# Performance work log

Measured on AMD Instinct MI355X. Metric: run time of the kernel, lower is better.

The kernel has to match this reference:

```python
import jax, jax.numpy as jnp
import numpy as np

N = 100000   # nodes
E = 640000   # edges
DIN = 128
DOUT = 128
BN_EPS = 1e-5


def setup_inputs() -> dict:
    key = jax.random.key(0)
    k = jax.random.split(key, 6)
    x = jax.random.normal(k[0], (N, DIN), dtype=jnp.float32)
    edge_index = jax.random.randint(k[1], (2, E), 0, N, dtype=jnp.int64)
    # MLP params: Linear(DIN,DOUT) -> BatchNorm1d(DOUT) -> ReLU -> Linear(DOUT,DOUT)
    s1 = 1.0 / np.sqrt(DIN)
    s2 = 1.0 / np.sqrt(DOUT)
    W1 = jax.random.uniform(k[2], (DIN, DOUT), jnp.float32, -s1, s1)
    b1 = jax.random.uniform(k[3], (DOUT,), jnp.float32, -s1, s1)
    gamma = jnp.ones((DOUT,), jnp.float32)
    beta = jnp.zeros((DOUT,), jnp.float32)
    W2 = jax.random.uniform(k[4], (DOUT, DOUT), jnp.float32, -s2, s2)
    b2 = jax.random.uniform(k[5], (DOUT,), jnp.float32, -s2, s2)
    eps = jnp.zeros((), jnp.float32)  # train_eps=True, init 0.0
    return {"x": x, "edge_index": edge_index, "W1": W1, "b1": b1,
            "gamma": gamma, "beta": beta, "W2": W2, "b2": b2, "eps": eps}


def reference(x, edge_index, W1, b1, gamma, beta, W2, b2, eps):
    src = edge_index[0]
    dst = edge_index[1]
    # GIN sum aggregation: gather source features, scatter-add to target nodes
    agg = jax.ops.segment_sum(x[src], dst, num_segments=N)  # [N, DIN]
    h = agg + (1.0 + eps) * x  # eps-weighted residual combine
    # MLP: Linear -> BatchNorm1d (training stats, biased var) -> ReLU -> Linear
    h = h @ W1 + b1  # [N, DOUT]
    mu = jnp.mean(h, axis=0)
    var = jnp.mean((h - mu) ** 2, axis=0)
    h = (h - mu) * jax.lax.rsqrt(var + BN_EPS) * gamma + beta
    h = jnp.maximum(h, 0.0)
    return h @ W2 + b2
```

## Files before the change

kernel.cpp:

```cpp
#include <hip/hip_runtime.h>

#define N_NODES 100000
#define DIM     128
#define NEDGE   640000
#define BN_EPS  1e-5f

#define PB_CNT  2500
#define PB_X    6250
#define PB_W    64

#define NSLOT   32
#define NBUCKET 64
#define T_TILES 4
#define GGRID   1563
#define AGRID   6250

typedef __bf16 bf16x8 __attribute__((ext_vector_type(8)));
typedef float  f32x4  __attribute__((ext_vector_type(4)));
typedef unsigned short u16x8 __attribute__((ext_vector_type(8)));

__device__ __forceinline__ unsigned short f2b(float f) {
    unsigned u = __builtin_bit_cast(unsigned, f);
    u += 0x7fffu + ((u >> 16) & 1u);
    return (unsigned short)(u >> 16);
}
__device__ __forceinline__ float b2f(unsigned short b) {
    return __builtin_bit_cast(float, ((unsigned)b) << 16);
}

__global__ __launch_bounds__(256) void k_prep(const float* __restrict__ x,
                                              const float* __restrict__ W1,
                                              const float* __restrict__ W2,
                                              const int* __restrict__ ei,
                                              unsigned short* __restrict__ xb,
                                              unsigned short* __restrict__ Wt1,
                                              unsigned short* __restrict__ Wt2,
                                              unsigned* __restrict__ cnt,
                                              int* __restrict__ slots) {
    const int b = blockIdx.x;
    const int t = threadIdx.x;
    if (b < PB_CNT) {
        int e = b * 256 + t;
        int src = ei[e];
        int dst = ei[NEDGE + e];
        unsigned r = (unsigned)e & 3u;
        #pragma unroll
        for (int a = 0; a < 4; ++a) {
            unsigned rk = atomicAdd(&cnt[dst * 4 + r], 1u);
            if (rk < 8u) {
                slots[dst * NSLOT + r * 8 + rk] = src;
                break;
            }
            r = (r + 1) & 3u;
        }
    } else if (b < PB_CNT + PB_X) {
        size_t base = ((size_t)(b - PB_CNT) * 256 + t) * 8;
        float4 v0 = *(const float4*)(x + base);
        float4 v1 = *(const float4*)(x + base + 4);
        u16x8 o;
        o[0] = f2b(v0.x); o[1] = f2b(v0.y); o[2] = f2b(v0.z); o[3] = f2b(v0.w);
        o[4] = f2b(v1.x); o[5] = f2b(v1.y); o[6] = f2b(v1.z); o[7] = f2b(v1.w);
        *(u16x8*)(xb + base) = o;
    } else if (b < PB_CNT + PB_X + PB_W) {
        int idx = (b - PB_CNT - PB_X) * 256 + t;
        int k = idx >> 7, n = idx & 127;
        Wt1[n * 128 + k] = f2b(W1[idx]);
    } else {
        int idx = (b - PB_CNT - PB_X - PB_W) * 256 + t;
        int k = idx >> 7, n = idx & 127;
        Wt2[n * 128 + k] = f2b(W2[idx]);
    }
}

__global__ __launch_bounds__(256) void k_agg1(const unsigned short* __restrict__ xb,
                                              const unsigned* __restrict__ cnt,
                                              const int* __restrict__ slots,
                                              const float* __restrict__ epsp,
                                              const unsigned short* __restrict__ Wt,
                                              const float* __restrict__ b1,
                                              unsigned short* __restrict__ hB,
                                              float* __restrict__ buckets) {
    __shared__ __align__(16) unsigned short At[16 * 136];
    __shared__ __align__(16) unsigned short stage[4][512];
    const int t = threadIdx.x;
    const int w = t >> 6;
    const int lane = t & 63;
    const int n15 = lane & 15;
    const int quad = lane >> 4;
    const int c8 = n15 * 8;
    const int gbase = lane & 48;

    const int row0 = blockIdx.x * 16;
    const int node = row0 + w * 4 + quad;

    int4 Bfr[2][4];
    const unsigned short* wp = Wt + (w * 32 + n15) * 128 + quad * 8;
    #pragma unroll
    for (int c = 0; c < 2; ++c)
        #pragma unroll
        for (int ks = 0; ks < 4; ++ks)
            Bfr[c][ks] = *(const int4*)(wp + c * 16 * 128 + ks * 32);
    float bias[2] = { b1[w * 32 + n15], b1[w * 32 + 16 + n15] };
    const float scale = 1.0f + epsp[0];

    const uint4 cw = *(const uint4*)(cnt + node * 4);
    const int s_lo = slots[node * NSLOT + n15];
    const int s_hi = slots[node * NSLOT + 16 + n15];
    float acc[8];
    {
        u16x8 v = *(const u16x8*)(xb + (size_t)node * 128 + c8);
        #pragma unroll
        for (int j = 0; j < 8; ++j) acc[j] = scale * b2f(v[j]);
    }
    unsigned m;
    {
        unsigned d0 = cw.x > 8u ? 8u : cw.x;
        unsigned d1 = cw.y > 8u ? 8u : cw.y;
        unsigned d2 = cw.z > 8u ? 8u : cw.z;
        unsigned d3 = cw.w > 8u ? 8u : cw.w;
        m = ((1u << d0) - 1u) | (((1u << d1) - 1u) << 8) |
            (((1u << d2) - 1u) << 16) | (((1u << d3) - 1u) << 24);
    }
    const int navail = __popc(m);
    unsigned mm = m;
    int pk = 0;
    for (int done = 0; done < navail; done += 8) {
        int4 va[8];
        #pragma unroll
        for (int k = 0; k < 8; ++k) {
            if (mm) { pk = (int)__builtin_ctz(mm); mm &= (mm - 1); }
            int vlo = __shfl(s_lo, gbase + (pk & 15));
            int vhi = __shfl(s_hi, gbase + (pk & 15));
            int srck = (pk & 16) ? vhi : vlo;
            va[k] = *(const int4*)(xb + (size_t)srck * 128 + c8);
        }
        const int rem = navail - done;
        #pragma unroll
        for (int k = 0; k < 8; ++k) {
            if (k < rem) {
                u16x8 v = __builtin_bit_cast(u16x8, va[k]);
                #pragma unroll
                for (int j = 0; j < 8; ++j) acc[j] += b2f(v[j]);
            }
        }
    }
    {
        u16x8 o;
        #pragma unroll
        for (int j = 0; j < 8; ++j) o[j] = f2b(acc[j]);
        *(u16x8*)(At + (w * 4 + quad) * 136 + c8) = o;
    }
    __syncthreads();

    f32x4 accm[2] = {};
    #pragma unroll
    for (int ks = 0; ks < 4; ++ks) {
        int4 araw = *(const int4*)(At + n15 * 136 + ks * 32 + quad * 8);
        bf16x8 af = __builtin_bit_cast(bf16x8, araw);
        #pragma unroll
        for (int c = 0; c < 2; ++c)
            accm[c] = __builtin_amdgcn_mfma_f32_16x16x32_bf16(
                af, __builtin_bit_cast(bf16x8, Bfr[c][ks]), accm[c], 0, 0, 0);
    }
    float s[2] = {0.f, 0.f}, q[2] = {0.f, 0.f};
    unsigned short* st = stage[w];
    #pragma unroll
    for (int c = 0; c < 2; ++c)
        #pragma unroll
        for (int r = 0; r < 4; ++r) {
            float v = accm[c][r] + bias[c];
            s[c] += v; q[c] += v * v;
            st[(quad * 4 + r) * 32 + c * 16 + n15] = f2b(v);
        }
    {
        int so = lane * 8;
        int r = so >> 5, cc = so & 31;
        *(int4*)(hB + (size_t)(row0 + r) * 128 + w * 32 + cc) = *(const int4*)(st + so);
    }

    #pragma unroll
    for (int c = 0; c < 2; ++c) {
        s[c] += __shfl_down(s[c], 32); q[c] += __shfl_down(q[c], 32);
        s[c] += __shfl_down(s[c], 16); q[c] += __shfl_down(q[c], 16);
    }
    if (quad == 0) {
        float* bk = buckets + (blockIdx.x & (NBUCKET - 1)) * 256;
        atomicAdd(&bk[w * 32 + n15], s[0]);
        atomicAdd(&bk[w * 32 + 16 + n15], s[1]);
        atomicAdd(&bk[128 + w * 32 + n15], q[0]);
        atomicAdd(&bk[128 + w * 32 + 16 + n15], q[1]);
    }
}

__global__ __launch_bounds__(256) void k_gemm2(const unsigned short* __restrict__ hb,
                                               const unsigned short* __restrict__ Wt2,
                                               const float* __restrict__ buckets,
                                               const float* __restrict__ gamma,
                                               const float* __restrict__ beta,
                                               const float* __restrict__ b2,
                                               float* __restrict__ out) {
    __shared__ __align__(16) unsigned short Asb[2][16 * 136];
    __shared__ __align__(16) float stage[4][512];
    __shared__ __align__(16) float aff_s[256];
    const int t = threadIdx.x;
    const int w = t >> 6;
    const int lane = t & 63;
    const int n15 = lane & 15;
    const int quad = lane >> 4;
    const int kb = w * 32 + quad * 8;

    const int tile0 = blockIdx.x * T_TILES;
    int4 gr;
    {
        int r0 = tile0 * 16;
        if (r0 < N_NODES)
            gr = *(const int4*)(hb + (size_t)(r0 + n15) * 128 + kb);
    }

    int4 Bfr[2][4];
    const unsigned short* wp = Wt2 + (w * 32 + n15) * 128 + quad * 8;
    #pragma unroll
    for (int c = 0; c < 2; ++c)
        #pragma unroll
        for (int ks = 0; ks < 4; ++ks)
            Bfr[c][ks] = *(const int4*)(wp + c * 16 * 128 + ks * 32);
    float bias[2] = { b2[w * 32 + n15], b2[w * 32 + 16 + n15] };

    if (t < 128) {
        float s = 0.f, q = 0.f;
        #pragma unroll 8
        for (int b = 0; b < NBUCKET; ++b) {
            s += buckets[b * 256 + t];
            q += buckets[b * 256 + 128 + t];
        }
        float mu  = s * (1.0f / N_NODES);
        float var = q * (1.0f / N_NODES) - mu * mu;
        float a = gamma[t] * rsqrtf(var + BN_EPS);
        aff_s[t] = a;
        aff_s[128 + t] = beta[t] - mu * a;
    }
    __syncthreads();

    float akr[8], bkr[8];
    *(float4*)(akr)     = *(const float4*)(aff_s + kb);
    *(float4*)(akr + 4) = *(const float4*)(aff_s + kb + 4);
    *(float4*)(bkr)     = *(const float4*)(aff_s + 128 + kb);
    *(float4*)(bkr + 4) = *(const float4*)(aff_s + 128 + kb + 4);

    float* st = stage[w];

    #pragma unroll
    for (int i = 0; i < T_TILES; ++i) {
        const int row0 = (tile0 + i) * 16;
        const bool valid = row0 < N_NODES;
        unsigned short* al = Asb[i & 1];
        if (valid) {
            u16x8 ar = __builtin_bit_cast(u16x8, gr);
            u16x8 pr;
            #pragma unroll
            for (int j = 0; j < 8; ++j)
                pr[j] = f2b(fmaxf(fmaf(b2f(ar[j]), akr[j], bkr[j]), 0.f));
            *(int4*)(al + n15 * 136 + kb) = __builtin_bit_cast(int4, pr);
        }
        if (i + 1 < T_TILES) {
            int rn = (tile0 + i + 1) * 16;
            if (rn < N_NODES)
                gr = *(const int4*)(hb + (size_t)(rn + n15) * 128 + kb);
        }
        __syncthreads();
        if (valid) {
            f32x4 acc[2] = {};
            #pragma unroll
            for (int ks = 0; ks < 4; ++ks) {
                int4 araw = *(const int4*)(al + n15 * 136 + ks * 32 + quad * 8);
                bf16x8 af = __builtin_bit_cast(bf16x8, araw);
                #pragma unroll
                for (int c = 0; c < 2; ++c)
                    acc[c] = __builtin_amdgcn_mfma_f32_16x16x32_bf16(
                        af, __builtin_bit_cast(bf16x8, Bfr[c][ks]), acc[c], 0, 0, 0);
            }
            #pragma unroll
            for (int c = 0; c < 2; ++c)
                #pragma unroll
                for (int r = 0; r < 4; ++r)
                    st[(quad * 4 + r) * 32 + c * 16 + n15] = acc[c][r] + bias[c];
            #pragma unroll
            for (int p = 0; p < 2; ++p) {
                int fo = p * 256 + lane * 4;
                int r = fo >> 5, cc = fo & 31;
                *(float4*)(out + (size_t)(row0 + r) * 128 + w * 32 + cc) =
                    *(const float4*)(st + fo);
            }
        }
    }
}

extern "C" void kernel_launch(void* const* d_in, const int* in_sizes, int n_in,
                              void* d_out, int out_size, void* d_ws, size_t ws_size,
                              hipStream_t stream) {
    const float* x     = (const float*)d_in[0];
    const int*   ei    = (const int*)d_in[1];
    const float* W1    = (const float*)d_in[2];
    const float* b1    = (const float*)d_in[3];
    const float* gamma = (const float*)d_in[4];
    const float* beta  = (const float*)d_in[5];
    const float* W2    = (const float*)d_in[6];
    const float* b2    = (const float*)d_in[7];
    const float* eps   = (const float*)d_in[8];
    float* out = (float*)d_out;

    float* buckets      = (float*)d_ws;
    unsigned* cnt       = (unsigned*)(buckets + NBUCKET * 256);
    unsigned short* hB  = (unsigned short*)(cnt + 4 * N_NODES);
    unsigned short* xb  = hB + (size_t)N_NODES * DIM;
    unsigned short* Wt1 = xb + (size_t)N_NODES * DIM;
    unsigned short* Wt2 = Wt1 + 16384;
    int* slots          = (int*)(Wt2 + 16384);

    hipMemsetAsync(buckets, 0,
                   NBUCKET * 256 * sizeof(float) + 4 * N_NODES * sizeof(unsigned),
                   stream);

    k_prep<<<PB_CNT + PB_X + 2 * PB_W, 256, 0, stream>>>(x, W1, W2, ei, xb, Wt1, Wt2,
                                                         cnt, slots);
    k_agg1<<<AGRID, 256, 0, stream>>>(xb, cnt, slots, eps, Wt1, b1, hB, buckets);
    k_gemm2<<<GGRID, 256, 0, stream>>>(hB, Wt2, buckets, gamma, beta, b2, out);
}
```

Measured before the change: 208.9 us.

## Split BN finalize into its own kernel, batch edge atomics, recoalesce gemm2 loads

The BatchNorm statistics reduction moves out of every k_gemm2 block into a single tiny k_finalize kernel that writes the affine coefficients to the workspace, so the 1563 gemm2 blocks no longer each re-read 64 buckets and wait on a block barrier. k_prep now has each thread handle two edges and issue both first-try atomics before resolving overflow with a helper. The helper allows only 3 tries after the first, so every slot can still be reached. k_gemm2 also changes its A-tile load so each lane reads 8 contiguous bf16 of a row (row-major coalesced) instead of the previous column-split layout, and drops the software prefetch of the next tile. This adds an extra kernel launch and loses the load/compute overlap.

```diff
diff --git a/kernel.cpp b/kernel.cpp
--- a/kernel.cpp
+++ b/kernel.cpp
@@ -5,7 +5,7 @@
 #define NEDGE   640000
 #define BN_EPS  1e-5f
 
-#define PB_CNT  2500
+#define PB_CNT2 1250
 #define PB_X    6250
 #define PB_W    64
 
@@ -26,6 +26,16 @@
 }
 __device__ __forceinline__ float b2f(unsigned short b) {
     return __builtin_bit_cast(float, ((unsigned)b) << 16);
+}
+
+__device__ __forceinline__ void claim_slot(unsigned* cnt, int* slots,
+                                           int dst, int src, unsigned r) {
+    #pragma unroll
+    for (int a = 0; a < 3; ++a) {
+        unsigned rk = atomicAdd(&cnt[dst * 4 + r], 1u);
+        if (rk < 8u) { slots[dst * NSLOT + r * 8 + rk] = src; return; }
+        r = (r + 1) & 3u;
+    }
 }
 
 __global__ __launch_bounds__(256) void k_prep(const float* __restrict__ x,
@@ -39,34 +49,33 @@
                                               int* __restrict__ slots) {
     const int b = blockIdx.x;
     const int t = threadIdx.x;
-    if (b < PB_CNT) {
-        int e = b * 256 + t;
-        int src = ei[e];
-        int dst = ei[NEDGE + e];
-        unsigned r = (unsigned)e & 3u;
-        #pragma unroll
-        for (int a = 0; a < 4; ++a) {
-            unsigned rk = atomicAdd(&cnt[dst * 4 + r], 1u);
-            if (rk < 8u) {
-                slots[dst * NSLOT + r * 8 + rk] = src;
-                break;
-            }
-            r = (r + 1) & 3u;
-        }
-    } else if (b < PB_CNT + PB_X) {
-        size_t base = ((size_t)(b - PB_CNT) * 256 + t) * 8;
+    if (b < PB_CNT2) {
+        int e0 = b * 512 + t;
+        int e1 = e0 + 256;
+        int src0 = ei[e0], src1 = ei[e1];
+        int dst0 = ei[NEDGE + e0], dst1 = ei[NEDGE + e1];
+        unsigned r0 = (unsigned)e0 & 3u;
+        unsigned r1 = (unsigned)e1 & 3u;
+        unsigned rk0 = atomicAdd(&cnt[dst0 * 4 + r0], 1u);
+        unsigned rk1 = atomicAdd(&cnt[dst1 * 4 + r1], 1u);
+        if (rk0 < 8u) slots[dst0 * NSLOT + r0 * 8 + rk0] = src0;
+        else          claim_slot(cnt, slots, dst0, src0, (r0 + 1) & 3u);
+        if (rk1 < 8u) slots[dst1 * NSLOT + r1 * 8 + rk1] = src1;
+        else          claim_slot(cnt, slots, dst1, src1, (r1 + 1) & 3u);
+    } else if (b < PB_CNT2 + PB_X) {
+        size_t base = ((size_t)(b - PB_CNT2) * 256 + t) * 8;
         float4 v0 = *(const float4*)(x + base);
         float4 v1 = *(const float4*)(x + base + 4);
         u16x8 o;
         o[0] = f2b(v0.x); o[1] = f2b(v0.y); o[2] = f2b(v0.z); o[3] = f2b(v0.w);
         o[4] = f2b(v1.x); o[5] = f2b(v1.y); o[6] = f2b(v1.z); o[7] = f2b(v1.w);
         *(u16x8*)(xb + base) = o;
-    } else if (b < PB_CNT + PB_X + PB_W) {
-        int idx = (b - PB_CNT - PB_X) * 256 + t;
+    } else if (b < PB_CNT2 + PB_X + PB_W) {
+        int idx = (b - PB_CNT2 - PB_X) * 256 + t;
         int k = idx >> 7, n = idx & 127;
         Wt1[n * 128 + k] = f2b(W1[idx]);
     } else {
-        int idx = (b - PB_CNT - PB_X - PB_W) * 256 + t;
+        int idx = (b - PB_CNT2 - PB_X - PB_W) * 256 + t;
         int k = idx >> 7, n = idx & 127;
         Wt2[n * 128 + k] = f2b(W2[idx]);
     }
@@ -192,30 +201,40 @@
     }
 }
 
+__global__ void k_finalize(const float* __restrict__ gamma,
+                           const float* __restrict__ beta,
+                           const float* __restrict__ buckets,
+                           float* __restrict__ aff) {
+    int c = threadIdx.x;
+    if (c < DIM) {
+        float s = 0.f, q = 0.f;
+        #pragma unroll 8
+        for (int b = 0; b < NBUCKET; ++b) {
+            s += buckets[b * 256 + c];
+            q += buckets[b * 256 + 128 + c];
+        }
+        float mu  = s * (1.0f / N_NODES);
+        float var = q * (1.0f / N_NODES) - mu * mu;
+        float a = gamma[c] * rsqrtf(var + BN_EPS);
+        aff[c] = a;
+        aff[DIM + c] = beta[c] - mu * a;
+    }
+}
+
 __global__ __launch_bounds__(256) void k_gemm2(const unsigned short* __restrict__ hb,
                                                const unsigned short* __restrict__ Wt2,
-                                               const float* __restrict__ buckets,
-                                               const float* __restrict__ gamma,
-                                               const float* __restrict__ beta,
+                                               const float* __restrict__ aff,
                                                const float* __restrict__ b2,
                                                float* __restrict__ out) {
     __shared__ __align__(16) unsigned short Asb[2][16 * 136];
     __shared__ __align__(16) float stage[4][512];
-    __shared__ __align__(16) float aff_s[256];
     const int t = threadIdx.x;
     const int w = t >> 6;
     const int lane = t & 63;
     const int n15 = lane & 15;
     const int quad = lane >> 4;
-    const int kb = w * 32 + quad * 8;
-
-    const int tile0 = blockIdx.x * T_TILES;
-    int4 gr;
-    {
-        int r0 = tile0 * 16;
-        if (r0 < N_NODES)
-            gr = *(const int4*)(hb + (size_t)(r0 + n15) * 128 + kb);
-    }
+    const int c8 = n15 * 8;
+    const int lrow = w * 4 + quad;
 
     int4 Bfr[2][4];
     const unsigned short* wp = Wt2 + (w * 32 + n15) * 128 + quad * 8;
@@ -224,29 +243,15 @@
         #pragma unroll
         for (int ks = 0; ks < 4; ++ks)
             Bfr[c][ks] = *(const int4*)(wp + c * 16 * 128 + ks * 32);
+
+    float akr[8], bkr[8];
+    *(float4*)(akr)     = *(const float4*)(aff + c8);
+    *(float4*)(akr + 4) = *(const float4*)(aff + c8 + 4);
+    *(float4*)(bkr)     = *(const float4*)(aff + 128 + c8);
+    *(float4*)(bkr + 4) = *(const float4*)(aff + 128 + c8 + 4);
     float bias[2] = { b2[w * 32 + n15], b2[w * 32 + 16 + n15] };
 
-    if (t < 128) {
-        float s = 0.f, q = 0.f;
-        #pragma unroll 8
-        for (int b = 0; b < NBUCKET; ++b) {
-            s += buckets[b * 256 + t];
-            q += buckets[b * 256 + 128 + t];
-        }
-        float mu  = s * (1.0f / N_NODES);
-        float var = q * (1.0f / N_NODES) - mu * mu;
-        float a = gamma[t] * rsqrtf(var + BN_EPS);
-        aff_s[t] = a;
-        aff_s[128 + t] = beta[t] - mu * a;
-    }
-    __syncthreads();
-
-    float akr[8], bkr[8];
-    *(float4*)(akr)     = *(const float4*)(aff_s + kb);
-    *(float4*)(akr + 4) = *(const float4*)(aff_s + kb + 4);
-    *(float4*)(bkr)     = *(const float4*)(aff_s + 128 + kb);
-    *(float4*)(bkr + 4) = *(const float4*)(aff_s + 128 + kb + 4);
-
+    const int tile0 = blockIdx.x * T_TILES;
     float* st = stage[w];
 
     #pragma unroll
@@ -255,17 +260,13 @@
         const bool valid = row0 < N_NODES;
         unsigned short* al = Asb[i & 1];
         if (valid) {
-            u16x8 ar = __builtin_bit_cast(u16x8, gr);
+            int4 graw = *(const int4*)(hb + (size_t)(row0 + lrow) * 128 + c8);
+            u16x8 ar = __builtin_bit_cast(u16x8, graw);
             u16x8 pr;
             #pragma unroll
             for (int j = 0; j < 8; ++j)
                 pr[j] = f2b(fmaxf(fmaf(b2f(ar[j]), akr[j], bkr[j]), 0.f));
-            *(int4*)(al + n15 * 136 + kb) = __builtin_bit_cast(int4, pr);
-        }
-        if (i + 1 < T_TILES) {
-            int rn = (tile0 + i + 1) * 16;
-            if (rn < N_NODES)
-                gr = *(const int4*)(hb + (size_t)(rn + n15) * 128 + kb);
+            *(int4*)(al + lrow * 136 + c8) = __builtin_bit_cast(int4, pr);
         }
         __syncthreads();
         if (valid) {
@@ -311,7 +312,8 @@
 
     float* buckets      = (float*)d_ws;
     unsigned* cnt       = (unsigned*)(buckets + NBUCKET * 256);
-    unsigned short* hB  = (unsigned short*)(cnt + 4 * N_NODES);
+    float* aff          = (float*)(cnt + 4 * N_NODES);
+    unsigned short* hB  = (unsigned short*)(aff + 256);
     unsigned short* xb  = hB + (size_t)N_NODES * DIM;
     unsigned short* Wt1 = xb + (size_t)N_NODES * DIM;
     unsigned short* Wt2 = Wt1 + 16384;
@@ -321,8 +323,9 @@
                    NBUCKET * 256 * sizeof(float) + 4 * N_NODES * sizeof(unsigned),
                    stream);
 
-    k_prep<<<PB_CNT + PB_X + 2 * PB_W, 256, 0, stream>>>(x, W1, W2, ei, xb, Wt1, Wt2,
-                                                         cnt, slots);
+    k_prep<<<PB_CNT2 + PB_X + 2 * PB_W, 256, 0, stream>>>(x, W1, W2, ei, xb, Wt1, Wt2,
+                                                          cnt, slots);
     k_agg1<<<AGRID, 256, 0, stream>>>(xb, cnt, slots, eps, Wt1, b1, hB, buckets);
-    k_gemm2<<<GGRID, 256, 0, stream>>>(hB, Wt2, buckets, gamma, beta, b2, out);
-}
+    k_finalize<<<1, 128, 0, stream>>>(gamma, beta, buckets, aff);
+    k_gemm2<<<GGRID, 256, 0, stream>>>(hB, Wt2, aff, b2, out);
+}
```

Measured after the change: 212.2 us. Within noise of the previous version (+1.6%).
